# Performance work log

Hardware: AMD Instinct MI355X
Metric: run time of the kernel (lower is better)

The kernel has to match this reference:

```python
import jax, jax.numpy as jnp
import numpy as np

NUM_POINTS = 200000
IN_FEATURES = 128
OUT_FEATURES = 128
NUM_RELATIONS = 128
NUM_BLOCKS = 16
IN_BLOCK = IN_FEATURES // NUM_BLOCKS   # 8
OUT_BLOCK = OUT_FEATURES // NUM_BLOCKS  # 8


def setup_inputs() -> dict:
    key = jax.random.key(0)
    k1, k2, k3 = jax.random.split(key, 3)
    x = jax.random.normal(k1, (NUM_POINTS, IN_FEATURES), dtype=jnp.float32)
    # glorot-uniform init of the per-relation block-diagonal weights
    blocks = jax.nn.initializers.glorot_uniform()(
        k2, (NUM_RELATIONS, NUM_BLOCKS, IN_BLOCK, OUT_BLOCK), jnp.float32)
    rel = jax.random.randint(k3, (NUM_POINTS,), 0, NUM_RELATIONS)
    return {"x": x, "blocks": blocks, "rel": rel}


def reference(x, blocks, rel):
    # x: [p, num_blocks*in_block]; blocks: [R, nb, ib, ob]; rel: [p] int
    p = x.shape[0]
    R, nb, ib, ob = blocks.shape
    x_by_block = x.reshape(p, nb, ib)                 # [p, nb, ib]
    relation_blocks = blocks[rel]                     # gather: [p, nb, ib, ob]
    transformed = jnp.einsum('pnio,pni->pno', relation_blocks, x_by_block)
    return transformed.reshape(p, nb * ob)            # [p, out_features]
```

## Files before the change

kernel.cpp:

```cpp
#include <hip/hip_runtime.h>


__device__ __forceinline__ float4 dpp_swap1(float4 v) {
    union { float4 f; int i[4]; } a, b;
    a.f = v;
    b.i[0] = __builtin_amdgcn_update_dpp(0, a.i[0], 0xB1, 0xF, 0xF, true);
    b.i[1] = __builtin_amdgcn_update_dpp(0, a.i[1], 0xB1, 0xF, 0xF, true);
    b.i[2] = __builtin_amdgcn_update_dpp(0, a.i[2], 0xB1, 0xF, 0xF, true);
    b.i[3] = __builtin_amdgcn_update_dpp(0, a.i[3], 0xB1, 0xF, 0xF, true);
    return b.f;
}

__global__ __launch_bounds__(1024) void k_fused(
    const float* __restrict__ x, const float* __restrict__ w,
    const int* __restrict__ rel, float* __restrict__ out, int npoints)
{
    __shared__ float4 wlds[128][64];

    const int q = blockIdx.x >> 6;
    const int b = blockIdx.x & 63;

    const float4* wsrc = reinterpret_cast<const float4*>(w);
    #pragma unroll
    for (int j = 0; j < 8; ++j) {
        int f  = threadIdx.x + j * 1024;
        int r  = f >> 6;
        int lo = f & 63;
        int nl = lo >> 4;
        int k  = f & 15;
        wlds[r][((k << 2) | nl) ^ (r & 63)] = wsrc[r * 256 + q * 64 + lo];
    }
    __syncthreads();

    const int lane = threadIdx.x & 63;
    const int wv   = threadIdx.x >> 6;
    const int pt8  = lane >> 3;
    const int j    = lane & 7;
    const int nl   = j >> 1;
    const int h    = j & 1;

    const int chunk = (npoints + 63) >> 6;
    const int plo = b * chunk;
    const int phi = min(plo + chunk, npoints);

    int g1 = plo + wv * 8;
    if (g1 >= phi) return;

    const float4* xv = reinterpret_cast<const float4*>(x) + q * 8 + j;
    float4*       ov = reinterpret_cast<float4*>(out) + q * 8 + j;

    int p1  = g1 + pt8;
    int p1c = min(p1, phi - 1);
    int r1  = rel[p1c];
    float4 xa1 = xv[(size_t)p1c * 32];

    int g2  = g1 + 128;
    int p2c = min(g2 + pt8, phi - 1);
    int r2  = rel[p2c];
    float4 xa2 = xv[(size_t)p2c * 32];

    while (true) {
        int g3  = g1 + 256;
        int p3c = min(g3 + pt8, phi - 1);
        int r3  = rel[p3c];
        float4 xa3 = xv[(size_t)p3c * 32];

        {
            float4 xo  = dpp_swap1(xa1);
            float4 xlo = h ? xo  : xa1;
            float4 xhi = h ? xa1 : xo;
            const int s   = r1 & 63;
            const int thi = s & 0x38;
            const int t0  = ((h << 2) | nl) ^ (s & 7);
            const float4* base = wlds[r1];
            float xf[8] = {xlo.x, xlo.y, xlo.z, xlo.w,
                           xhi.x, xhi.y, xhi.z, xhi.w};
            float a0 = 0.f, a1 = 0.f, a2 = 0.f, a3 = 0.f;
            #pragma unroll
            for (int i = 0; i < 8; ++i) {
                float4 wv4 = base[((i << 3) ^ thi) | t0];
                float xi = xf[i];
                a0 = fmaf(xi, wv4.x, a0);
                a1 = fmaf(xi, wv4.y, a1);
                a2 = fmaf(xi, wv4.z, a2);
                a3 = fmaf(xi, wv4.w, a3);
            }
            if (p1 < phi)
                ov[(size_t)p1 * 32] = make_float4(a0, a1, a2, a3);
        }

        if (g2 >= phi) break;
        g1 = g2; p1 = g1 + pt8; r1 = r2; xa1 = xa2;
        g2 = g3;                r2 = r3; xa2 = xa3;
    }
}

__global__ __launch_bounds__(256) void brl_kernel(
    const float* __restrict__ x, const float* __restrict__ w,
    const int* __restrict__ rel, float* __restrict__ out, int npoints)
{
    int tid = blockIdx.x * 256 + threadIdx.x;
    int p = tid >> 4;
    if (p >= npoints) return;
    int n = tid & 15;
    int r = rel[p];
    const float4* xv = reinterpret_cast<const float4*>(x + (size_t)p * 128 + n * 8);
    float4 x0 = xv[0], x1 = xv[1];
    float xf[8] = {x0.x, x0.y, x0.z, x0.w, x1.x, x1.y, x1.z, x1.w};
    const float4* wv = reinterpret_cast<const float4*>(w + ((size_t)r * 16 + n) * 64);
    float acc[8] = {0.f, 0.f, 0.f, 0.f, 0.f, 0.f, 0.f, 0.f};
    #pragma unroll
    for (int i = 0; i < 8; ++i) {
        float4 w0 = wv[2 * i], w1 = wv[2 * i + 1];
        float wf[8] = {w0.x, w0.y, w0.z, w0.w, w1.x, w1.y, w1.z, w1.w};
        #pragma unroll
        for (int o = 0; o < 8; ++o) acc[o] = fmaf(xf[i], wf[o], acc[o]);
    }
    float4* ov = reinterpret_cast<float4*>(out + (size_t)p * 128 + n * 8);
    ov[0] = make_float4(acc[0], acc[1], acc[2], acc[3]);
    ov[1] = make_float4(acc[4], acc[5], acc[6], acc[7]);
}

extern "C" void kernel_launch(void* const* d_in, const int* in_sizes, int n_in,
                              void* d_out, int out_size, void* d_ws, size_t ws_size,
                              hipStream_t stream) {
    const float* x   = (const float*)d_in[0];
    const float* w   = (const float*)d_in[1];
    const int*   rel = (const int*)d_in[2];
    float*       out = (float*)d_out;

    int npoints = in_sizes[2];
    int R = in_sizes[1] / 1024;

    if (R == 128 && in_sizes[0] == npoints * 128) {
        k_fused<<<256, 1024, 0, stream>>>(x, w, rel, out, npoints);
    } else {
        int total = npoints * 16;
        brl_kernel<<<(total + 255) / 256, 256, 0, stream>>>(x, w, rel, out, npoints);
    }
}
```

Baseline: 190.5 us.

## Process four point-groups per wave iteration with batched prefetch and nontemporal stores

Each wave now handles 32 consecutive points per iteration, four groups of 8, instead of one group of 8. It prefetches the next iteration's four x/rel loads as a batch, so more global loads are in flight per wave. Output writes switch to nontemporal stores to avoid polluting cache with streamed results. This costs more registers, and the coarser granularity may leave waves idle at chunk tails.

```diff
diff --git a/kernel.cpp b/kernel.cpp
--- a/kernel.cpp
+++ b/kernel.cpp
@@ -1,5 +1,7 @@
 #include <hip/hip_runtime.h>
 
+
+typedef float v4f __attribute__((ext_vector_type(4)));
 
 __device__ __forceinline__ float4 dpp_swap1(float4 v) {
     union { float4 f; int i[4]; } a, b;
@@ -22,13 +24,13 @@
 
     const float4* wsrc = reinterpret_cast<const float4*>(w);
     #pragma unroll
-    for (int j = 0; j < 8; ++j) {
-        int f  = threadIdx.x + j * 1024;
-        int r  = f >> 6;
-        int lo = f & 63;
-        int nl = lo >> 4;
-        int k  = f & 15;
-        wlds[r][((k << 2) | nl) ^ (r & 63)] = wsrc[r * 256 + q * 64 + lo];
+    for (int t = 0; t < 8; ++t) {
+        int f   = threadIdx.x + t * 1024;
+        int r   = f >> 6;
+        int lo  = f & 63;
+        int nls = lo >> 4;
+        int k   = f & 15;
+        wlds[r][((k << 2) | nls) ^ (r & 63)] = wsrc[r * 256 + q * 64 + lo];
     }
     __syncthreads();
 
@@ -40,58 +42,78 @@
     const int h    = j & 1;
 
     const int chunk = (npoints + 63) >> 6;
-    const int plo = b * chunk;
-    const int phi = min(plo + chunk, npoints);
+    const int plo   = b * chunk;
+    const int phi   = min(plo + chunk, npoints);
+    const int phim1 = phi - 1;
 
-    int g1 = plo + wv * 8;
-    if (g1 >= phi) return;
+    int gB = plo + wv * 32;
+    if (gB >= phi) return;
 
     const float4* xv = reinterpret_cast<const float4*>(x) + q * 8 + j;
     float4*       ov = reinterpret_cast<float4*>(out) + q * 8 + j;
 
-    int p1  = g1 + pt8;
-    int p1c = min(p1, phi - 1);
-    int r1  = rel[p1c];
-    float4 xa1 = xv[(size_t)p1c * 32];
+    auto comp = [&](int r1, float4 xa, int p1) {
+        float4 xo  = dpp_swap1(xa);
+        float4 xlo = h ? xo  : xa;
+        float4 xhi = h ? xa : xo;
+        const int s   = r1 & 63;
+        const int thi = s & 0x38;
+        const int t0  = ((h << 2) | nl) ^ (s & 7);
+        const float4* base = wlds[r1];
+        float xf[8] = {xlo.x, xlo.y, xlo.z, xlo.w,
+                       xhi.x, xhi.y, xhi.z, xhi.w};
+        float a0 = 0.f, a1 = 0.f, a2 = 0.f, a3 = 0.f;
+        #pragma unroll
+        for (int i = 0; i < 8; ++i) {
+            float4 wv4 = base[((i << 3) ^ thi) | t0];
+            float xi = xf[i];
+            a0 = fmaf(xi, wv4.x, a0);
+            a1 = fmaf(xi, wv4.y, a1);
+            a2 = fmaf(xi, wv4.z, a2);
+            a3 = fmaf(xi, wv4.w, a3);
+        }
+        if (p1 < phi) {
+            v4f val = {a0, a1, a2, a3};
+            __builtin_nontemporal_store(val,
+                reinterpret_cast<v4f*>(&ov[(size_t)p1 * 32]));
+        }
+    };
 
-    int g2  = g1 + 128;
-    int p2c = min(g2 + pt8, phi - 1);
-    int r2  = rel[p2c];
-    float4 xa2 = xv[(size_t)p2c * 32];
+    int    rr0, rr1, rr2, rr3;
+    float4 xr0, xr1, xr2, xr3;
+    {
+        int p0 = min(gB +  0 + pt8, phim1);
+        int p1 = min(gB +  8 + pt8, phim1);
+        int p2 = min(gB + 16 + pt8, phim1);
+        int p3 = min(gB + 24 + pt8, phim1);
+        rr0 = rel[p0]; rr1 = rel[p1]; rr2 = rel[p2]; rr3 = rel[p3];
+        xr0 = xv[(size_t)p0 * 32]; xr1 = xv[(size_t)p1 * 32];
+        xr2 = xv[(size_t)p2 * 32]; xr3 = xv[(size_t)p3 * 32];
+    }
 
     while (true) {
-        int g3  = g1 + 256;
-        int p3c = min(g3 + pt8, phi - 1);
-        int r3  = rel[p3c];
-        float4 xa3 = xv[(size_t)p3c * 32];
-
-        {
-            float4 xo  = dpp_swap1(xa1);
-            float4 xlo = h ? xo  : xa1;
-            float4 xhi = h ? xa1 : xo;
-            const int s   = r1 & 63;
-            const int thi = s & 0x38;
-            const int t0  = ((h << 2) | nl) ^ (s & 7);
-            const float4* base = wlds[r1];
-            float xf[8] = {xlo.x, xlo.y, xlo.z, xlo.w,
-                           xhi.x, xhi.y, xhi.z, xhi.w};
-            float a0 = 0.f, a1 = 0.f, a2 = 0.f, a3 = 0.f;
-            #pragma unroll
-            for (int i = 0; i < 8; ++i) {
-                float4 wv4 = base[((i << 3) ^ thi) | t0];
-                float xi = xf[i];
-                a0 = fmaf(xi, wv4.x, a0);
-                a1 = fmaf(xi, wv4.y, a1);
-                a2 = fmaf(xi, wv4.z, a2);
-                a3 = fmaf(xi, wv4.w, a3);
-            }
-            if (p1 < phi)
-                ov[(size_t)p1 * 32] = make_float4(a0, a1, a2, a3);
+        int gN = gB + 512;
+        int    rn0, rn1, rn2, rn3;
+        float4 xn0, xn1, xn2, xn3;
+        if (gN < phi) {
+            int p0 = min(gN +  0 + pt8, phim1);
+            int p1 = min(gN +  8 + pt8, phim1);
+            int p2 = min(gN + 16 + pt8, phim1);
+            int p3 = min(gN + 24 + pt8, phim1);
+            xn0 = xv[(size_t)p0 * 32]; xn1 = xv[(size_t)p1 * 32];
+            xn2 = xv[(size_t)p2 * 32]; xn3 = xv[(size_t)p3 * 32];
+            rn0 = rel[p0]; rn1 = rel[p1]; rn2 = rel[p2]; rn3 = rel[p3];
         }
 
-        if (g2 >= phi) break;
-        g1 = g2; p1 = g1 + pt8; r1 = r2; xa1 = xa2;
-        g2 = g3;                r2 = r3; xa2 = xa3;
+        comp(rr0, xr0, gB +  0 + pt8);
+        comp(rr1, xr1, gB +  8 + pt8);
+        comp(rr2, xr2, gB + 16 + pt8);
+        comp(rr3, xr3, gB + 24 + pt8);
+
+        if (gN >= phi) break;
+        gB = gN;
+        rr0 = rn0; rr1 = rn1; rr2 = rn2; rr3 = rn3;
+        xr0 = xn0; xr1 = xn1; xr2 = xn2; xr3 = xn3;
     }
 }
 
```

Result: slower. 195.7 us (+2.7%).
